# Kernel optimization log

Measured on AMD Instinct MI355X. Metric: run time of the kernel, lower is better.

The kernel has to match this reference:

```python
import jax, jax.numpy as jnp
import numpy as np

DIM_Q = 1024
DIM_K = 1024
DIM_V = 1024


def setup_inputs() -> dict:
    key = jax.random.key(0)
    kx, kq, kk, kv = jax.random.split(key, 4)
    x = jax.random.normal(kx, (4, 2048, DIM_Q), dtype=jnp.float32)
    # torch nn.Linear weights: [out_features, in_features], y = x @ W.T
    scale = 1.0 / np.sqrt(DIM_Q)
    Wq = jax.random.uniform(kq, (DIM_K, DIM_Q), dtype=jnp.float32, minval=-scale, maxval=scale)
    Wk = jax.random.uniform(kk, (DIM_K, DIM_Q), dtype=jnp.float32, minval=-scale, maxval=scale)
    Wv = jax.random.uniform(kv, (DIM_V, DIM_Q), dtype=jnp.float32, minval=-scale, maxval=scale)
    return {"x": x, "Wq": Wq, "Wk": Wk, "Wv": Wv}


def reference(x, Wq, Wk, Wv):
    # q, k: [b, s, dim_k]; v: [b, s, dim_v]
    q = jnp.einsum('bsd,kd->bsk', x, Wq)
    k = jnp.einsum('bsd,kd->bsk', x, Wk)
    v = jnp.einsum('bsd,vd->bsv', x, Wv)
    norm_fact = 1.0 / jnp.sqrt(jnp.asarray(DIM_K, dtype=x.dtype))
    score = jnp.einsum('bik,bjk->bij', q, k) * norm_fact  # [b, s, s]
    score = jax.nn.softmax(score, axis=-1)
    att = jnp.einsum('bij,bjv->biv', score, v)
    att = att + v  # is_residual=True
    return att
```

## Files before the change

### kernel.cpp

```cpp
#include <hip/hip_runtime.h>
#include <hip/hip_bf16.h>

using bf16 = __hip_bfloat16;
typedef __attribute__((ext_vector_type(8))) short short8;
typedef __attribute__((ext_vector_type(4))) float floatx4;
typedef __attribute__((ext_vector_type(8))) int int8v;

__device__ __forceinline__ void async_ld16(const void* g, void* l) {
  __builtin_amdgcn_global_load_lds((const __attribute__((address_space(1))) void*)g,
                                   (__attribute__((address_space(3))) void*)l, 16, 0, 0);
}

__device__ __forceinline__ int pk4_fp8(float a, float b, float c, float d) {
  int v = __builtin_amdgcn_cvt_pk_fp8_f32(a, b, 0, false);
  return __builtin_amdgcn_cvt_pk_fp8_f32(c, d, v, true);
}

__device__ __forceinline__ void gemm_core(const bf16* __restrict__ At,
                                          const bf16* __restrict__ Bt,
                                          int K, bf16* lA, bf16* lB,
                                          floatx4 acc[4][4]) {
  const int tid  = threadIdx.x;
  const int w    = tid >> 6;
  const int lane = tid & 63;
  const int subM = (w >> 1) * 64;
  const int subN = (w & 1) * 64;
  const int fr   = lane & 15;
  const int fq   = lane >> 4;

  int srow[4], scol[4], sdst[4];
#pragma unroll
  for (int q = 0; q < 4; ++q) {
    int p = q * 256 + w * 64 + lane;
    int r = p >> 3;
    int j = (p & 7) ^ (r & 7);
    srow[q] = r;
    scol[q] = j * 8;
    sdst[q] = (q * 256 + w * 64) * 8;
  }
  int offA[2][4], offB[2][4];
#pragma unroll
  for (int kc = 0; kc < 2; ++kc)
#pragma unroll
    for (int i = 0; i < 4; ++i) {
      int rA = subM + i * 16 + fr;
      offA[kc][i] = (rA * 8 + ((kc * 4 + fq) ^ (rA & 7))) * 8;
      int rB = subN + i * 16 + fr;
      offB[kc][i] = (rB * 8 + ((kc * 4 + fq) ^ (rB & 7))) * 8;
    }

  floatx4 zero = {0.f, 0.f, 0.f, 0.f};
#pragma unroll
  for (int i = 0; i < 4; ++i)
#pragma unroll
    for (int j = 0; j < 4; ++j) acc[i][j] = zero;

  for (int k0 = 0; k0 < K; k0 += 64) {
    __syncthreads();
#pragma unroll
    for (int q = 0; q < 4; ++q) {
      async_ld16(At + (size_t)srow[q] * K + k0 + scol[q], lA + sdst[q]);
      async_ld16(Bt + (size_t)srow[q] * K + k0 + scol[q], lB + sdst[q]);
    }
    __syncthreads();
#pragma unroll
    for (int kc = 0; kc < 2; ++kc) {
      short8 a[4], b[4];
#pragma unroll
      for (int i = 0; i < 4; ++i) a[i] = *(const short8*)(lA + offA[kc][i]);
#pragma unroll
      for (int j = 0; j < 4; ++j) b[j] = *(const short8*)(lB + offB[kc][j]);
#pragma unroll
      for (int i = 0; i < 4; ++i)
#pragma unroll
        for (int j = 0; j < 4; ++j)
          acc[i][j] = __builtin_amdgcn_mfma_f32_16x16x32_bf16(a[i], b[j], acc[i][j], 0, 0, 0);
    }
  }
}

__device__ __forceinline__ void gemm_core_f8(const unsigned char* __restrict__ At,
                                             const unsigned char* __restrict__ Bt,
                                             int K, unsigned char* lA, unsigned char* lB,
                                             floatx4 acc[4][4]) {
  const int tid  = threadIdx.x;
  const int w    = tid >> 6;
  const int lane = tid & 63;
  const int subM = (w >> 1) * 64;
  const int subN = (w & 1) * 64;
  const int fr   = lane & 15;
  const int fq   = lane >> 4;

  int srow[4], scol[4], sdst[4];
#pragma unroll
  for (int q = 0; q < 4; ++q) {
    int p = q * 256 + w * 64 + lane;
    int r = p >> 3;
    int j = (p & 7) ^ (r & 7);
    srow[q] = r;
    scol[q] = j * 16;
    sdst[q] = (q * 256 + w * 64) * 16;
  }
  int offA[2][4], offB[2][4];
#pragma unroll
  for (int h = 0; h < 2; ++h)
#pragma unroll
    for (int i = 0; i < 4; ++i) {
      int rA = subM + i * 16 + fr;
      offA[h][i] = rA * 128 + (((fq * 2 + h) ^ (rA & 7)) * 16);
      int rB = subN + i * 16 + fr;
      offB[h][i] = rB * 128 + (((fq * 2 + h) ^ (rB & 7)) * 16);
    }

  floatx4 zero = {0.f, 0.f, 0.f, 0.f};
#pragma unroll
  for (int i = 0; i < 4; ++i)
#pragma unroll
    for (int j = 0; j < 4; ++j) acc[i][j] = zero;

  for (int k0 = 0; k0 < K; k0 += 128) {
    __syncthreads();
#pragma unroll
    for (int q = 0; q < 4; ++q) {
      async_ld16(At + (size_t)srow[q] * K + k0 + scol[q], lA + sdst[q]);
      async_ld16(Bt + (size_t)srow[q] * K + k0 + scol[q], lB + sdst[q]);
    }
    __syncthreads();
    int8v a[4], b[4];
#pragma unroll
    for (int i = 0; i < 4; ++i) {
      int4 lo = *(const int4*)(lA + offA[0][i]);
      int4 hi = *(const int4*)(lA + offA[1][i]);
      int8v v;
      v[0] = lo.x; v[1] = lo.y; v[2] = lo.z; v[3] = lo.w;
      v[4] = hi.x; v[5] = hi.y; v[6] = hi.z; v[7] = hi.w;
      a[i] = v;
    }
#pragma unroll
    for (int j = 0; j < 4; ++j) {
      int4 lo = *(const int4*)(lB + offB[0][j]);
      int4 hi = *(const int4*)(lB + offB[1][j]);
      int8v v;
      v[0] = lo.x; v[1] = lo.y; v[2] = lo.z; v[3] = lo.w;
      v[4] = hi.x; v[5] = hi.y; v[6] = hi.z; v[7] = hi.w;
      b[j] = v;
    }
#pragma unroll
    for (int i = 0; i < 4; ++i)
#pragma unroll
      for (int j = 0; j < 4; ++j)
        acc[i][j] = __builtin_amdgcn_mfma_scale_f32_16x16x128_f8f6f4(
            a[i], b[j], acc[i][j], 0, 0, 0, 0x7F7F7F7F, 0, 0x7F7F7F7F);
  }
}

__global__ __launch_bounds__(256) void v_gemm(const bf16* __restrict__ Xbf,
                                              const bf16* __restrict__ Wvbf,
                                              bf16* __restrict__ Vbf) {
  __shared__ bf16 lA[128 * 64];
  __shared__ bf16 lB[128 * 64];
  const int id = blockIdx.x;
  const int r = id & 7, g = id >> 3;
  const int ty = r * 8 + (g & 7);
  const int tx = g >> 3;

  const bf16* At = Xbf + (size_t)ty * 128 * 1024;
  const bf16* Bt = Wvbf + (size_t)tx * 128 * 1024;
  floatx4 acc[4][4];
  gemm_core(At, Bt, 1024, lA, lB, acc);

  const int tid = threadIdx.x, w = tid >> 6, lane = tid & 63;
  const int subM = (w >> 1) * 64, subN = (w & 1) * 64;
  const int fr = lane & 15, fq = lane >> 4;
  const int rowBase = ty * 128 + subM;
  const int colBase = tx * 128 + subN;
#pragma unroll
  for (int i = 0; i < 4; ++i)
#pragma unroll
    for (int j = 0; j < 4; ++j)
#pragma unroll
      for (int rr = 0; rr < 4; ++rr) {
        int row = rowBase + i * 16 + fq * 4 + rr;
        int col = colBase + j * 16 + fr;
        Vbf[(size_t)row * 1024 + col] = __float2bfloat16(acc[i][j][rr]);
      }
}

__global__ __launch_bounds__(256) void qk_proj_gemm(const unsigned char* __restrict__ X8,
                                                    const unsigned char* __restrict__ Wq8,
                                                    const unsigned char* __restrict__ Wk8,
                                                    unsigned char* __restrict__ Qf8,
                                                    unsigned char* __restrict__ Kf8) {
  __shared__ unsigned char lA[128 * 128];
  __shared__ unsigned char lB[128 * 128];
  const int id = blockIdx.x;
  const int r = id & 7, g = id >> 3;
  const int ty = r * 8 + (g & 7);
  const int tx = (g >> 3) & 7;
  const int z = g >> 6;

  const unsigned char* At = X8 + (size_t)ty * 128 * 1024;
  const unsigned char* Bt = (z == 0 ? Wq8 : Wk8) + (size_t)tx * 128 * 1024;
  floatx4 acc[4][4];
  gemm_core_f8(At, Bt, 1024, lA, lB, acc);

  unsigned char* dst = (z == 0) ? Qf8 : Kf8;
  const int tid = threadIdx.x, w = tid >> 6, lane = tid & 63;
  const int subM = (w >> 1) * 64, subN = (w & 1) * 64;
  const int fr = lane & 15, fq = lane >> 4;
  const int rowBase = ty * 128 + subM;
  const int colBase = tx * 128 + subN;
#pragma unroll
  for (int i = 0; i < 4; ++i)
#pragma unroll
    for (int rr = 0; rr < 4; ++rr) {
      int row = rowBase + i * 16 + fq * 4 + rr;
      int p = pk4_fp8(acc[0][0][0] * 0 + acc[i][0][rr], acc[i][1][rr],
                      acc[i][2][rr], acc[i][3][rr]);
#pragma unroll
      for (int j = 0; j < 4; ++j)
        dst[(size_t)row * 1024 + colBase + j * 16 + fr] = (unsigned char)(p >> (8 * j));
    }
}

__global__ __launch_bounds__(256) void transpose_v(const bf16* __restrict__ Vbf,
                                                   unsigned char* __restrict__ Vt8) {
  __shared__ short tile[64][72];
  const int b = blockIdx.z;
  const int s0 = blockIdx.x * 64;
  const int v0 = blockIdx.y * 64;
  const int t = threadIdx.x;
#pragma unroll
  for (int i = 0; i < 2; ++i) {
    int c = t + i * 256;
    int row = c >> 3, cj = c & 7;
    *(short8*)&tile[row][cj * 8] =
        *(const short8*)&Vbf[((size_t)(b * 2048 + s0 + row)) * 1024 + v0 + cj * 8];
  }
  __syncthreads();
  const int vrow = t >> 2, sq = t & 3;
#pragma unroll
  for (int hc = 0; hc < 2; ++hc) {
    float f[8];
#pragma unroll
    for (int e = 0; e < 8; ++e) {
      short s = tile[sq * 16 + hc * 8 + e][vrow];
      f[e] = __bfloat162float(*(bf16*)&s);
    }
    uint2 packed;
    packed.x = (unsigned int)pk4_fp8(f[0], f[1], f[2], f[3]);
    packed.y = (unsigned int)pk4_fp8(f[4], f[5], f[6], f[7]);
    *(uint2*)&Vt8[((size_t)(b * 1024 + v0 + vrow)) * 2048 + s0 + sq * 16 + hc * 8] = packed;
  }
}

__global__ __launch_bounds__(256) void qk_exp_gemm(const unsigned char* __restrict__ Qf8,
                                                   const unsigned char* __restrict__ Kf8,
                                                   unsigned char* __restrict__ S8,
                                                   float* __restrict__ l) {
  __shared__ unsigned char lA[128 * 128];
  __shared__ unsigned char lB[128 * 128];
  const int id = blockIdx.x;
  const int r = id & 7, g = id >> 3;
  const int b = g >> 5;
  const int rem = g & 31;
  const int ty = r * 2 + (rem & 1);
  const int tx = rem >> 1;

  const unsigned char* At = Qf8 + (size_t)b * 2048 * 1024 + (size_t)ty * 128 * 1024;
  const unsigned char* Bt = Kf8 + (size_t)b * 2048 * 1024 + (size_t)tx * 128 * 1024;
  floatx4 acc[4][4];
  gemm_core_f8(At, Bt, 1024, lA, lB, acc);

  const int tid = threadIdx.x, w = tid >> 6, lane = tid & 63;
  const int subM = (w >> 1) * 64, subN = (w & 1) * 64;
  const int fr = lane & 15, fq = lane >> 4;
  const int rowBase = ty * 128 + subM;
  const int colBase = tx * 128 + subN;
  unsigned char* Sb = S8 + (size_t)b * 2048 * 2048;
  float* lb = l + (size_t)b * 2048;
#pragma unroll
  for (int i = 0; i < 4; ++i)
#pragma unroll
    for (int rr = 0; rr < 4; ++rr) {
      int row = rowBase + i * 16 + fq * 4 + rr;
      int p = pk4_fp8(__expf(acc[i][0][rr] * 0.03125f), __expf(acc[i][1][rr] * 0.03125f),
                      __expf(acc[i][2][rr] * 0.03125f), __expf(acc[i][3][rr] * 0.03125f));
      float psum = __builtin_amdgcn_cvt_f32_fp8(p, 0) + __builtin_amdgcn_cvt_f32_fp8(p, 1) +
                   __builtin_amdgcn_cvt_f32_fp8(p, 2) + __builtin_amdgcn_cvt_f32_fp8(p, 3);
#pragma unroll
      for (int j = 0; j < 4; ++j)
        Sb[(size_t)row * 2048 + colBase + j * 16 + fr] = (unsigned char)(p >> (8 * j));
      psum += __shfl_xor(psum, 1, 64);
      psum += __shfl_xor(psum, 2, 64);
      psum += __shfl_xor(psum, 4, 64);
      psum += __shfl_xor(psum, 8, 64);
      if (fr == 0) atomicAdd(&lb[row], psum);
    }
}

__global__ __launch_bounds__(256) void pv_gemm(const unsigned char* __restrict__ S8,
                                               const unsigned char* __restrict__ Vt8,
                                               const bf16* __restrict__ Vbf,
                                               const float* __restrict__ l,
                                               float* __restrict__ out) {
  __shared__ unsigned char lA[128 * 128];
  __shared__ unsigned char lB[128 * 128];
  const int id = blockIdx.x;
  const int r = id & 7, g = id >> 3;
  const int b = g >> 4;
  const int rem = g & 15;
  const int ty = r * 2 + (rem & 1);
  const int tx = rem >> 1;

  const unsigned char* At = S8 + (size_t)b * 2048 * 2048 + (size_t)ty * 128 * 2048;
  const unsigned char* Bt = Vt8 + (size_t)b * 1024 * 2048 + (size_t)tx * 128 * 2048;
  floatx4 acc[4][4];
  gemm_core_f8(At, Bt, 2048, lA, lB, acc);

  const int tid = threadIdx.x, w = tid >> 6, lane = tid & 63;
  const int subM = (w >> 1) * 64, subN = (w & 1) * 64;
  const int fr = lane & 15, fq = lane >> 4;
  const int rowBase = ty * 128 + subM;
  const int colBase = tx * 128 + subN;
  const float* lb = l + (size_t)b * 2048;
#pragma unroll
  for (int i = 0; i < 4; ++i)
#pragma unroll
    for (int rr = 0; rr < 4; ++rr) {
      int row = rowBase + i * 16 + fq * 4 + rr;
      float inv = 1.0f / lb[row];
#pragma unroll
      for (int j = 0; j < 4; ++j) {
        int col = colBase + j * 16 + fr;
        size_t oi = ((size_t)b * 2048 + row) * 1024 + col;
        out[oi] = acc[i][j][rr] * inv + __bfloat162float(Vbf[oi]);
      }
    }
}

__global__ void cast_all(const float* __restrict__ x, const float* __restrict__ wq,
                         const float* __restrict__ wk, const float* __restrict__ wv,
                         bf16* __restrict__ Xbf, unsigned char* __restrict__ X8,
                         unsigned char* __restrict__ Wq8, unsigned char* __restrict__ Wk8,
                         bf16* __restrict__ Wvbf, float* __restrict__ l) {
  const int blk = blockIdx.x;
  const int t = threadIdx.x;
  if (blk < 8192) {
    int i = blk * 256 + t;
    float4 f = ((const float4*)x)[i];
    bf16 tmp[4] = {__float2bfloat16(f.x), __float2bfloat16(f.y),
                   __float2bfloat16(f.z), __float2bfloat16(f.w)};
    ((ushort4*)Xbf)[i] = *(const ushort4*)tmp;
    ((unsigned int*)X8)[i] = (unsigned int)pk4_fp8(f.x, f.y, f.z, f.w);
  } else if (blk < 10240) {
    const float* src = (blk < 9216) ? wq : wk;
    unsigned char* dst = (blk < 9216) ? Wq8 : Wk8;
    int i = ((blk - 8192) & 1023) * 256 + t;
    float4 f = ((const float4*)src)[i];
    ((unsigned int*)dst)[i] = (unsigned int)pk4_fp8(f.x, f.y, f.z, f.w);
  } else if (blk < 11264) {
    int i = (blk - 10240) * 256 + t;
    float4 f = ((const float4*)wv)[i];
    bf16 tmp[4] = {__float2bfloat16(f.x), __float2bfloat16(f.y),
                   __float2bfloat16(f.z), __float2bfloat16(f.w)};
    ((ushort4*)Wvbf)[i] = *(const ushort4*)tmp;
  } else {
    int i = (blk - 11264) * 256 + t;
    ((float4*)l)[i] = make_float4(0.f, 0.f, 0.f, 0.f);
  }
}

extern "C" void kernel_launch(void* const* d_in, const int* in_sizes, int n_in,
                              void* d_out, int out_size, void* d_ws, size_t ws_size,
                              hipStream_t stream) {
  const float* x  = (const float*)d_in[0];
  const float* Wq = (const float*)d_in[1];
  const float* Wk = (const float*)d_in[2];
  const float* Wv = (const float*)d_in[3];
  float* out = (float*)d_out;

  char* ws = (char*)d_ws;
  bf16* Xbf = (bf16*)ws;                   ws += (size_t)8192 * 1024 * 2;
  unsigned char* X8 = (unsigned char*)ws;  ws += (size_t)8192 * 1024;
  unsigned char* Wq8 = (unsigned char*)ws; ws += (size_t)1024 * 1024;
  unsigned char* Wk8 = (unsigned char*)ws; ws += (size_t)1024 * 1024;
  bf16* Wvbf = (bf16*)ws;                  ws += (size_t)1024 * 1024 * 2;
  unsigned char* Qf8 = (unsigned char*)ws; ws += (size_t)8192 * 1024;
  unsigned char* Kf8 = (unsigned char*)ws; ws += (size_t)8192 * 1024;
  bf16* Vbf = (bf16*)ws;                   ws += (size_t)8192 * 1024 * 2;
  unsigned char* Vt8 = (unsigned char*)ws; ws += (size_t)4 * 1024 * 2048;
  unsigned char* S8  = (unsigned char*)ws; ws += (size_t)4 * 2048 * 2048;
  float* l = (float*)ws;                   ws += (size_t)8192 * 4;

  cast_all<<<11272, 256, 0, stream>>>(x, Wq, Wk, Wv, Xbf, X8, Wq8, Wk8, Wvbf, l);
  v_gemm<<<512, 256, 0, stream>>>(Xbf, Wvbf, Vbf);
  qk_proj_gemm<<<1024, 256, 0, stream>>>(X8, Wq8, Wk8, Qf8, Kf8);
  transpose_v<<<dim3(32, 16, 4), 256, 0, stream>>>(Vbf, Vt8);
  qk_exp_gemm<<<1024, 256, 0, stream>>>(Qf8, Kf8, S8, l);
  pv_gemm<<<512, 256, 0, stream>>>(S8, Vt8, Vbf, l, out);
}
```

Before: 199.5 us.

## Merge projection and mid-stage kernels; pack FP8 stores via permuted column layout

Cuts the launch sequence from five kernels to three. The V projection and the Q/K FP8 projections now run in one grid, and the QK-exp GEMM and the V transpose run in another, using block-index branching and a shared LDS buffer. The FP8 epilogues now write one 4-byte packed word per row chunk instead of four single-byte stores. This permutes the columns of Q, K and S inside each 64-wide group. The V transpose applies the matching permutation so that S·V stays correct. The aim is to cut launch gaps and tail idle time and to make stores cheaper, at the cost of heterogeneous blocks within a grid and a more fragile hidden layout contract.

```diff
diff --git a/kernel.cpp b/kernel.cpp
--- a/kernel.cpp
+++ b/kernel.cpp
@@ -15,6 +15,7 @@
   int v = __builtin_amdgcn_cvt_pk_fp8_f32(a, b, 0, false);
   return __builtin_amdgcn_cvt_pk_fp8_f32(c, d, v, true);
 }
+
 
 __device__ __forceinline__ void gemm_core(const bf16* __restrict__ At,
                                           const bf16* __restrict__ Bt,
@@ -154,149 +155,137 @@
   }
 }
 
-__global__ __launch_bounds__(256) void v_gemm(const bf16* __restrict__ Xbf,
-                                              const bf16* __restrict__ Wvbf,
-                                              bf16* __restrict__ Vbf) {
-  __shared__ bf16 lA[128 * 64];
-  __shared__ bf16 lB[128 * 64];
+__global__ __launch_bounds__(256) void proj_gemm(
+    const bf16* __restrict__ Xbf, const bf16* __restrict__ Wvbf, bf16* __restrict__ Vbf,
+    const unsigned char* __restrict__ X8, const unsigned char* __restrict__ Wq8,
+    const unsigned char* __restrict__ Wk8,
+    unsigned char* __restrict__ Qf8, unsigned char* __restrict__ Kf8) {
+  __shared__ __align__(16) char lds[32768];
   const int id = blockIdx.x;
-  const int r = id & 7, g = id >> 3;
-  const int ty = r * 8 + (g & 7);
-  const int tx = g >> 3;
-
-  const bf16* At = Xbf + (size_t)ty * 128 * 1024;
-  const bf16* Bt = Wvbf + (size_t)tx * 128 * 1024;
-  floatx4 acc[4][4];
-  gemm_core(At, Bt, 1024, lA, lB, acc);
-
   const int tid = threadIdx.x, w = tid >> 6, lane = tid & 63;
   const int subM = (w >> 1) * 64, subN = (w & 1) * 64;
   const int fr = lane & 15, fq = lane >> 4;
-  const int rowBase = ty * 128 + subM;
-  const int colBase = tx * 128 + subN;
-#pragma unroll
-  for (int i = 0; i < 4; ++i)
-#pragma unroll
-    for (int j = 0; j < 4; ++j)
+
+  if (id < 512) {
+    const int r = id & 7, g = id >> 3;
+    const int ty = r * 8 + (g & 7), tx = g >> 3;
+    bf16* lA = (bf16*)lds;
+    bf16* lB = (bf16*)(lds + 16384);
+    floatx4 acc[4][4];
+    gemm_core(Xbf + (size_t)ty * 128 * 1024, Wvbf + (size_t)tx * 128 * 1024,
+              1024, lA, lB, acc);
+    const int rowBase = ty * 128 + subM;
+    const int colBase = tx * 128 + subN;
+#pragma unroll
+    for (int i = 0; i < 4; ++i)
+#pragma unroll
+      for (int j = 0; j < 4; ++j)
+#pragma unroll
+        for (int rr = 0; rr < 4; ++rr) {
+          int row = rowBase + i * 16 + fq * 4 + rr;
+          int col = colBase + j * 16 + fr;
+          Vbf[(size_t)row * 1024 + col] = __float2bfloat16(acc[i][j][rr]);
+        }
+  } else {
+    const int local = id - 512;
+    const int z = local >> 9, lid = local & 511;
+    const int r = lid & 7, g = lid >> 3;
+    const int ty = r * 8 + (g & 7), tx = g >> 3;
+    unsigned char* lA = (unsigned char*)lds;
+    unsigned char* lB = (unsigned char*)(lds + 16384);
+    floatx4 acc[4][4];
+    gemm_core_f8(X8 + (size_t)ty * 128 * 1024,
+                 (z == 0 ? Wq8 : Wk8) + (size_t)tx * 128 * 1024, 1024, lA, lB, acc);
+    unsigned char* dst = (z == 0) ? Qf8 : Kf8;
+    const int rowBase = ty * 128 + subM;
+    const int colBase = tx * 128 + subN;
+#pragma unroll
+    for (int i = 0; i < 4; ++i)
 #pragma unroll
       for (int rr = 0; rr < 4; ++rr) {
         int row = rowBase + i * 16 + fq * 4 + rr;
-        int col = colBase + j * 16 + fr;
-        Vbf[(size_t)row * 1024 + col] = __float2bfloat16(acc[i][j][rr]);
+        unsigned int p = (unsigned int)pk4_fp8(acc[i][0][rr], acc[i][1][rr],
+                                               acc[i][2][rr], acc[i][3][rr]);
+        *(unsigned int*)&dst[(size_t)row * 1024 + colBase + fr * 4] = p;
       }
-}
-
-__global__ __launch_bounds__(256) void qk_proj_gemm(const unsigned char* __restrict__ X8,
-                                                    const unsigned char* __restrict__ Wq8,
-                                                    const unsigned char* __restrict__ Wk8,
-                                                    unsigned char* __restrict__ Qf8,
-                                                    unsigned char* __restrict__ Kf8) {
-  __shared__ unsigned char lA[128 * 128];
-  __shared__ unsigned char lB[128 * 128];
+  }
+}
+
+__global__ __launch_bounds__(256) void mid_kernel(
+    const unsigned char* __restrict__ Qf8, const unsigned char* __restrict__ Kf8,
+    unsigned char* __restrict__ S8, float* __restrict__ l,
+    const bf16* __restrict__ Vbf, unsigned char* __restrict__ Vt8) {
+  __shared__ __align__(16) char lds[32768];
   const int id = blockIdx.x;
-  const int r = id & 7, g = id >> 3;
-  const int ty = r * 8 + (g & 7);
-  const int tx = (g >> 3) & 7;
-  const int z = g >> 6;
-
-  const unsigned char* At = X8 + (size_t)ty * 128 * 1024;
-  const unsigned char* Bt = (z == 0 ? Wq8 : Wk8) + (size_t)tx * 128 * 1024;
-  floatx4 acc[4][4];
-  gemm_core_f8(At, Bt, 1024, lA, lB, acc);
-
-  unsigned char* dst = (z == 0) ? Qf8 : Kf8;
-  const int tid = threadIdx.x, w = tid >> 6, lane = tid & 63;
-  const int subM = (w >> 1) * 64, subN = (w & 1) * 64;
-  const int fr = lane & 15, fq = lane >> 4;
-  const int rowBase = ty * 128 + subM;
-  const int colBase = tx * 128 + subN;
-#pragma unroll
-  for (int i = 0; i < 4; ++i)
-#pragma unroll
-    for (int rr = 0; rr < 4; ++rr) {
-      int row = rowBase + i * 16 + fq * 4 + rr;
-      int p = pk4_fp8(acc[0][0][0] * 0 + acc[i][0][rr], acc[i][1][rr],
-                      acc[i][2][rr], acc[i][3][rr]);
-#pragma unroll
-      for (int j = 0; j < 4; ++j)
-        dst[(size_t)row * 1024 + colBase + j * 16 + fr] = (unsigned char)(p >> (8 * j));
-    }
-}
-
-__global__ __launch_bounds__(256) void transpose_v(const bf16* __restrict__ Vbf,
-                                                   unsigned char* __restrict__ Vt8) {
-  __shared__ short tile[64][72];
-  const int b = blockIdx.z;
-  const int s0 = blockIdx.x * 64;
-  const int v0 = blockIdx.y * 64;
   const int t = threadIdx.x;
-#pragma unroll
-  for (int i = 0; i < 2; ++i) {
-    int c = t + i * 256;
-    int row = c >> 3, cj = c & 7;
-    *(short8*)&tile[row][cj * 8] =
-        *(const short8*)&Vbf[((size_t)(b * 2048 + s0 + row)) * 1024 + v0 + cj * 8];
-  }
-  __syncthreads();
-  const int vrow = t >> 2, sq = t & 3;
-#pragma unroll
-  for (int hc = 0; hc < 2; ++hc) {
-    float f[8];
-#pragma unroll
-    for (int e = 0; e < 8; ++e) {
-      short s = tile[sq * 16 + hc * 8 + e][vrow];
-      f[e] = __bfloat162float(*(bf16*)&s);
-    }
-    uint2 packed;
-    packed.x = (unsigned int)pk4_fp8(f[0], f[1], f[2], f[3]);
-    packed.y = (unsigned int)pk4_fp8(f[4], f[5], f[6], f[7]);
-    *(uint2*)&Vt8[((size_t)(b * 1024 + v0 + vrow)) * 2048 + s0 + sq * 16 + hc * 8] = packed;
-  }
-}
-
-__global__ __launch_bounds__(256) void qk_exp_gemm(const unsigned char* __restrict__ Qf8,
-                                                   const unsigned char* __restrict__ Kf8,
-                                                   unsigned char* __restrict__ S8,
-                                                   float* __restrict__ l) {
-  __shared__ unsigned char lA[128 * 128];
-  __shared__ unsigned char lB[128 * 128];
-  const int id = blockIdx.x;
-  const int r = id & 7, g = id >> 3;
-  const int b = g >> 5;
-  const int rem = g & 31;
-  const int ty = r * 2 + (rem & 1);
-  const int tx = rem >> 1;
-
-  const unsigned char* At = Qf8 + (size_t)b * 2048 * 1024 + (size_t)ty * 128 * 1024;
-  const unsigned char* Bt = Kf8 + (size_t)b * 2048 * 1024 + (size_t)tx * 128 * 1024;
-  floatx4 acc[4][4];
-  gemm_core_f8(At, Bt, 1024, lA, lB, acc);
-
-  const int tid = threadIdx.x, w = tid >> 6, lane = tid & 63;
-  const int subM = (w >> 1) * 64, subN = (w & 1) * 64;
-  const int fr = lane & 15, fq = lane >> 4;
-  const int rowBase = ty * 128 + subM;
-  const int colBase = tx * 128 + subN;
-  unsigned char* Sb = S8 + (size_t)b * 2048 * 2048;
-  float* lb = l + (size_t)b * 2048;
-#pragma unroll
-  for (int i = 0; i < 4; ++i)
-#pragma unroll
-    for (int rr = 0; rr < 4; ++rr) {
-      int row = rowBase + i * 16 + fq * 4 + rr;
-      int p = pk4_fp8(__expf(acc[i][0][rr] * 0.03125f), __expf(acc[i][1][rr] * 0.03125f),
-                      __expf(acc[i][2][rr] * 0.03125f), __expf(acc[i][3][rr] * 0.03125f));
-      float psum = __builtin_amdgcn_cvt_f32_fp8(p, 0) + __builtin_amdgcn_cvt_f32_fp8(p, 1) +
-                   __builtin_amdgcn_cvt_f32_fp8(p, 2) + __builtin_amdgcn_cvt_f32_fp8(p, 3);
-#pragma unroll
-      for (int j = 0; j < 4; ++j)
-        Sb[(size_t)row * 2048 + colBase + j * 16 + fr] = (unsigned char)(p >> (8 * j));
-      psum += __shfl_xor(psum, 1, 64);
-      psum += __shfl_xor(psum, 2, 64);
-      psum += __shfl_xor(psum, 4, 64);
-      psum += __shfl_xor(psum, 8, 64);
-      if (fr == 0) atomicAdd(&lb[row], psum);
-    }
+
+  if (id < 1024) {
+    const int r = id & 7, g = id >> 3;
+    const int b = g >> 5;
+    const int rem = g & 31;
+    const int ty = r * 2 + (rem & 1);
+    const int tx = rem >> 1;
+    unsigned char* lA = (unsigned char*)lds;
+    unsigned char* lB = (unsigned char*)(lds + 16384);
+    floatx4 acc[4][4];
+    gemm_core_f8(Qf8 + (size_t)b * 2048 * 1024 + (size_t)ty * 128 * 1024,
+                 Kf8 + (size_t)b * 2048 * 1024 + (size_t)tx * 128 * 1024,
+                 1024, lA, lB, acc);
+    const int w = t >> 6, lane = t & 63;
+    const int subM = (w >> 1) * 64, subN = (w & 1) * 64;
+    const int fr = lane & 15, fq = lane >> 4;
+    const int rowBase = ty * 128 + subM;
+    const int colBase = tx * 128 + subN;
+    unsigned char* Sb = S8 + (size_t)b * 2048 * 2048;
+    float* lb = l + (size_t)b * 2048;
+#pragma unroll
+    for (int i = 0; i < 4; ++i)
+#pragma unroll
+      for (int rr = 0; rr < 4; ++rr) {
+        int row = rowBase + i * 16 + fq * 4 + rr;
+        unsigned int p = (unsigned int)pk4_fp8(
+            __expf(acc[i][0][rr] * 0.03125f), __expf(acc[i][1][rr] * 0.03125f),
+            __expf(acc[i][2][rr] * 0.03125f), __expf(acc[i][3][rr] * 0.03125f));
+        *(unsigned int*)&Sb[(size_t)row * 2048 + colBase + fr * 4] = p;
+        float psum = __builtin_amdgcn_cvt_f32_fp8(p, 0) + __builtin_amdgcn_cvt_f32_fp8(p, 1) +
+                     __builtin_amdgcn_cvt_f32_fp8(p, 2) + __builtin_amdgcn_cvt_f32_fp8(p, 3);
+        psum += __shfl_xor(psum, 1, 64);
+        psum += __shfl_xor(psum, 2, 64);
+        psum += __shfl_xor(psum, 4, 64);
+        psum += __shfl_xor(psum, 8, 64);
+        if (fr == 0) atomicAdd(&lb[row], psum);
+      }
+  } else {
+    const int t2 = id - 1024;
+    const int b = t2 >> 9, rem = t2 & 511;
+    const int xs = rem & 31, yv = rem >> 5;
+    const int s0 = xs * 64, v0 = yv * 64;
+    short(*tile)[72] = (short(*)[72])lds;
+#pragma unroll
+    for (int i = 0; i < 2; ++i) {
+      int c = t + i * 256;
+      int row = c >> 3, cj = c & 7;
+      *(short8*)&tile[row][cj * 8] =
+          *(const short8*)&Vbf[((size_t)(b * 2048 + s0 + row)) * 1024 + v0 + cj * 8];
+    }
+    __syncthreads();
+    const int vrow = t >> 2, sq = t & 3;
+#pragma unroll
+    for (int hc = 0; hc < 2; ++hc) {
+      float f[8];
+#pragma unroll
+      for (int e = 0; e < 8; ++e) {
+        int p = sq * 16 + hc * 8 + e;
+        int s = (p & 3) * 16 + (p >> 2);
+        short sh = tile[s][vrow];
+        f[e] = __bfloat162float(*(bf16*)&sh);
+      }
+      uint2 packed;
+      packed.x = (unsigned int)pk4_fp8(f[0], f[1], f[2], f[3]);
+      packed.y = (unsigned int)pk4_fp8(f[4], f[5], f[6], f[7]);
+      *(uint2*)&Vt8[((size_t)(b * 1024 + v0 + vrow)) * 2048 + s0 + sq * 16 + hc * 8] = packed;
+    }
+  }
 }
 
 __global__ __launch_bounds__(256) void pv_gemm(const unsigned char* __restrict__ S8,
@@ -304,8 +293,9 @@
                                                const bf16* __restrict__ Vbf,
                                                const float* __restrict__ l,
                                                float* __restrict__ out) {
-  __shared__ unsigned char lA[128 * 128];
-  __shared__ unsigned char lB[128 * 128];
+  __shared__ __align__(16) char lds[32768];
+  unsigned char* lA = (unsigned char*)lds;
+  unsigned char* lB = (unsigned char*)(lds + 16384);
   const int id = blockIdx.x;
   const int r = id & 7, g = id >> 3;
   const int b = g >> 4;
@@ -313,10 +303,10 @@
   const int ty = r * 2 + (rem & 1);
   const int tx = rem >> 1;
 
-  const unsigned char* At = S8 + (size_t)b * 2048 * 2048 + (size_t)ty * 128 * 2048;
-  const unsigned char* Bt = Vt8 + (size_t)b * 1024 * 2048 + (size_t)tx * 128 * 2048;
   floatx4 acc[4][4];
-  gemm_core_f8(At, Bt, 2048, lA, lB, acc);
+  gemm_core_f8(S8 + (size_t)b * 2048 * 2048 + (size_t)ty * 128 * 2048,
+               Vt8 + (size_t)b * 1024 * 2048 + (size_t)tx * 128 * 2048,
+               2048, lA, lB, acc);
 
   const int tid = threadIdx.x, w = tid >> 6, lane = tid & 63;
   const int subM = (w >> 1) * 64, subN = (w & 1) * 64;
@@ -394,9 +384,7 @@
   float* l = (float*)ws;                   ws += (size_t)8192 * 4;
 
   cast_all<<<11272, 256, 0, stream>>>(x, Wq, Wk, Wv, Xbf, X8, Wq8, Wk8, Wvbf, l);
-  v_gemm<<<512, 256, 0, stream>>>(Xbf, Wvbf, Vbf);
-  qk_proj_gemm<<<1024, 256, 0, stream>>>(X8, Wq8, Wk8, Qf8, Kf8);
-  transpose_v<<<dim3(32, 16, 4), 256, 0, stream>>>(Vbf, Vt8);
-  qk_exp_gemm<<<1024, 256, 0, stream>>>(Qf8, Kf8, S8, l);
+  proj_gemm<<<1536, 256, 0, stream>>>(Xbf, Wvbf, Vbf, X8, Wq8, Wk8, Qf8, Kf8);
+  mid_kernel<<<3072, 256, 0, stream>>>(Qf8, Kf8, S8, l, Vbf, Vt8);
   pv_gemm<<<512, 256, 0, stream>>>(S8, Vt8, Vbf, l, out);
 }
```

Result: faster. 188.1 us (-5.7%).
